# Performance work log

Hardware: AMD Instinct MI355X
Metric: run time of the kernel (lower is better)

## Reference

```python
import jax, jax.numpy as jnp
import numpy as np

D_ATOM, D_MODEL, H = 128, 512, 4
D_H = D_ATOM // H
D_FF = 4 * D_ATOM
EPS = 1e-5


def _ln(x, g, b):
    m = jnp.mean(x, axis=-1, keepdims=True)
    v = jnp.mean((x - m) ** 2, axis=-1, keepdims=True)
    return (x - m) / jnp.sqrt(v + EPS) * g + b


def setup_inputs() -> dict:
    key = jax.random.key(0)
    ks = jax.random.split(key, 20)
    B, N_ATOM, N_PAIRS, N_TOK = 2, 2048, 16384, 512
    c_atom = jax.random.normal(ks[0], (B, N_ATOM, D_ATOM), dtype=jnp.float32)
    p_lm = jax.random.normal(ks[1], (B, N_PAIRS, 16), dtype=jnp.float32)
    p_lm_idx = jax.random.randint(ks[2], (B, N_PAIRS, 2), 0, N_ATOM, dtype=jnp.int32)
    token_idx = jnp.sort(jax.random.randint(ks[3], (B, N_ATOM), 0, N_TOK, dtype=jnp.int32), axis=-1)
    s = 0.05
    w = lambda k, sh: jax.random.normal(k, sh, dtype=jnp.float32) * s
    return {
        'c_atom': c_atom, 'p_lm': p_lm, 'p_lm_idx': p_lm_idx,
        'token_idx': token_idx, 'n_tokens': N_TOK,
        'ln_attn_g': jnp.ones((D_ATOM,), jnp.float32), 'ln_attn_b': jnp.zeros((D_ATOM,), jnp.float32),
        'w_q': w(ks[4], (D_ATOM, D_ATOM)), 'w_k': w(ks[5], (D_ATOM, D_ATOM)),
        'w_v': w(ks[6], (D_ATOM, D_ATOM)), 'w_g': w(ks[7], (D_ATOM, D_ATOM)),
        'w_o': w(ks[8], (D_ATOM, D_ATOM)),
        'pb_w': w(ks[9], (16, H)), 'pb_b': jnp.zeros((H,), jnp.float32),
        'ln_ff_g': jnp.ones((D_ATOM,), jnp.float32), 'ln_ff_b': jnp.zeros((D_ATOM,), jnp.float32),
        'sw_w1': w(ks[10], (D_ATOM, D_FF)), 'sw_w2': w(ks[11], (D_ATOM, D_FF)),
        'sw_w3': w(ks[12], (D_FF, D_ATOM)),
        'tok_w': w(ks[13], (D_ATOM, D_MODEL)), 'tok_b': jnp.zeros((D_MODEL,), jnp.float32),
    }


def reference(c_atom, p_lm, p_lm_idx, token_idx, n_tokens,
              ln_attn_g, ln_attn_b, w_q, w_k, w_v, w_g, w_o, pb_w, pb_b,
              ln_ff_g, ln_ff_b, sw_w1, sw_w2, sw_w3, tok_w, tok_b):
    B, N, _ = c_atom.shape
    q_n = _ln(c_atom, ln_attn_g, ln_attn_b)
    Q = (q_n @ w_q).reshape(B, N, H, D_H)
    K = (q_n @ w_k).reshape(B, N, H, D_H)
    V = (q_n @ w_v).reshape(B, N, H, D_H)
    G = q_n @ w_g  # (B, N, d_atom)

    scores = jnp.einsum('bihd,bjhd->bhij', Q, K) / jnp.sqrt(jnp.float32(D_H))

    bias = p_lm @ pb_w + pb_b  # (B, P, H)
    def scat(src, dst, b_):
        return jnp.zeros((H, N, N), b_.dtype).at[:, src, dst].set(b_.T)
    pair_bias = jax.vmap(scat)(p_lm_idx[..., 0], p_lm_idx[..., 1], bias)
    scores = scores + pair_bias

    token_mask = token_idx[:, :, None] == token_idx[:, None, :]  # (B,N,N)
    scores = jnp.where(token_mask[:, None], scores, -jnp.inf)
    attn = jax.nn.softmax(scores, axis=-1)
    attn = jnp.nan_to_num(attn)

    att_out = jnp.einsum('bhij,bjhd->bihd', attn, V).reshape(B, N, D_ATOM)
    q = c_atom + jax.nn.sigmoid(G) * (att_out @ w_o)
    h = _ln(q, ln_ff_g, ln_ff_b)
    q = q + (jax.nn.silu(h @ sw_w1) * (h @ sw_w2)) @ sw_w3
    atom_feat = q @ tok_w + tok_b  # (B, N, d_model)

    seg = (token_idx + jnp.arange(B, dtype=token_idx.dtype)[:, None] * n_tokens).reshape(-1)
    sums = jax.ops.segment_sum(atom_feat.reshape(B * N, D_MODEL), seg, num_segments=B * n_tokens)
    cnts = jax.ops.segment_sum(jnp.ones((B * N,), atom_feat.dtype), seg, num_segments=B * n_tokens)
    out = sums / jnp.maximum(cnts, 1.0)[:, None]
    return out.reshape(B, n_tokens, D_MODEL)
```

## Files before the change

kernel.cpp:

```cpp
#include <hip/hip_runtime.h>
#include <hip/hip_bf16.h>
#include <math.h>

#define B_     2
#define N_     2048
#define DA     128
#define H_     4
#define DH     32
#define DFF    512
#define DM     512
#define NT     512
#define NP     16384
#define MAXL   32
#define LDSP   136

typedef short bf16x8 __attribute__((ext_vector_type(8)));
typedef float f32x4  __attribute__((ext_vector_type(4)));

__device__ __forceinline__ short bf16r(float x) {
    union { float f; unsigned u; } v; v.f = x;
    unsigned r = v.u + 0x7FFFu + ((v.u >> 16) & 1u);
    return (short)(r >> 16);
}
__device__ __forceinline__ float bf2f(short h) {
    union { unsigned u; float f; } v;
    v.u = ((unsigned)(unsigned short)h) << 16;
    return v.f;
}

__global__ __launch_bounds__(1024) void setup_kernel(
        const float* __restrict__ wq, const float* __restrict__ wk,
        const float* __restrict__ wv, const float* __restrict__ wg,
        const float* __restrict__ wo, const float* __restrict__ w1,
        const float* __restrict__ w2, const float* __restrict__ w3,
        const float* __restrict__ tw, const int* __restrict__ tok,
        const int* __restrict__ pidx,
        short* __restrict__ pqkvg, short* __restrict__ pwo,
        short* __restrict__ pw12, short* __restrict__ pw3,
        short* __restrict__ ptok,
        int* __restrict__ cnt, int* __restrict__ tst,
        int* __restrict__ win) {
    __shared__ int c[1024];
    __shared__ int sb[1024];
    if (blockIdx.x < 42) {
        int gid = blockIdx.x * 1024 + threadIdx.x;
        int lane = gid & 63;
        int grp = gid >> 6;
        int quad = lane >> 4, nn = lane & 15;
        const float* src; short* dst; int stride;
        if (grp < 128) {
            int g = grp; int kt = g & 3, nt = g >> 2;
            int n = nt * 16 + nn;
            const float* w = (n < 128) ? wq : (n < 256) ? wk : (n < 384) ? wv : wg;
            src = w + (kt * 32 + quad * 8) * 128 + (n & 127);
            dst = pqkvg + (g * 64 + lane) * 8;
            stride = 128;
        } else if (grp < 160) {
            int g = grp - 128; int kt = g & 3, nt = g >> 2;
            src = wo + (kt * 32 + quad * 8) * 128 + nt * 16 + nn;
            dst = pwo + (g * 64 + lane) * 8;
            stride = 128;
        } else if (grp < 416) {
            int g = grp - 160; int kt = g & 3, nt = g >> 2;
            int n = nt * 16 + nn;
            src = ((n & 1) ? w2 : w1) + (kt * 32 + quad * 8) * 512 + (n >> 1);
            dst = pw12 + (g * 64 + lane) * 8;
            stride = 512;
        } else if (grp < 544) {
            int g = grp - 416; int kt = g & 15, nt = g >> 4;
            src = w3 + (kt * 32 + quad * 8) * 128 + nt * 16 + nn;
            dst = pw3 + (g * 64 + lane) * 8;
            stride = 128;
        } else {
            int g = grp - 544; int kt = g & 3, nt = g >> 2;
            src = tw + (kt * 32 + quad * 8) * 512 + nt * 16 + nn;
            dst = ptok + (g * 64 + lane) * 8;
            stride = 512;
        }
#pragma unroll
        for (int j = 0; j < 8; j++) dst[j] = bf16r(src[j * stride]);
    } else if (blockIdx.x == 42) {
        int tid = threadIdx.x;
        c[tid] = 0;
        __syncthreads();
#pragma unroll
        for (int i = 0; i < 4; i++) {
            int idx = tid + i * 1024;
            int b = idx >> 11;
            atomicAdd(&c[b * NT + tok[idx]], 1);
        }
        __syncthreads();
        int t = tid & (NT - 1);
        int v = c[tid];
        int* cur = c;
        int* alt = sb;
        for (int d = 1; d < NT; d <<= 1) {
            int y = cur[tid];
            if (t >= d) y += cur[tid - d];
            alt[tid] = y;
            __syncthreads();
            int* tmp = cur; cur = alt; alt = tmp;
        }
        tst[tid] = cur[tid] - v;
        cnt[tid] = v;
    } else {
        int p = (blockIdx.x - 43) * 1024 + threadIdx.x;
        int b = p >> 14, pp = p & (NP - 1);
        int src = pidx[p * 2], dst = pidx[p * 2 + 1];
        if (tok[b * N_ + src] == tok[b * N_ + dst])
            atomicMax(&win[(b * N_ + src) * MAXL + (dst & 31)], pp + 1);
    }
}

__device__ __forceinline__ void ln_to_lds(const float* __restrict__ x,
                                          const float* __restrict__ g,
                                          const float* __restrict__ b,
                                          short* __restrict__ lds) {
    int t = threadIdx.x;
    int row = t >> 2, sub = t & 3;
    const float* xr = x + row * DA + sub * 32;
    float4 v[8];
    float s = 0.f, sq = 0.f;
#pragma unroll
    for (int i = 0; i < 8; i++) {
        v[i] = *(const float4*)(xr + i * 4);
        s  += v[i].x + v[i].y + v[i].z + v[i].w;
        sq += v[i].x * v[i].x + v[i].y * v[i].y + v[i].z * v[i].z + v[i].w * v[i].w;
    }
    s += __shfl_xor(s, 1); sq += __shfl_xor(sq, 1);
    s += __shfl_xor(s, 2); sq += __shfl_xor(sq, 2);
    float mean = s * (1.f / 128.f);
    float var = sq * (1.f / 128.f) - mean * mean;
    float inv = rsqrtf(var + 1e-5f);
    const float* gp = g + sub * 32;
    const float* bp = b + sub * 32;
    short* dst = lds + row * LDSP + sub * 32;
#pragma unroll
    for (int i = 0; i < 8; i++) {
        dst[i * 4 + 0] = bf16r((v[i].x - mean) * inv * gp[i * 4 + 0] + bp[i * 4 + 0]);
        dst[i * 4 + 1] = bf16r((v[i].y - mean) * inv * gp[i * 4 + 1] + bp[i * 4 + 1]);
        dst[i * 4 + 2] = bf16r((v[i].z - mean) * inv * gp[i * 4 + 2] + bp[i * 4 + 2]);
        dst[i * 4 + 3] = bf16r((v[i].w - mean) * inv * gp[i * 4 + 3] + bp[i * 4 + 3]);
    }
}

template<int K, int NTT>
__device__ __forceinline__ void gemm_lds(const short* __restrict__ Alds,
                                         const short* __restrict__ Bp,
                                         int nt0, int lane, f32x4* acc) {
    constexpr int KT = K / 32;
    const short* arow = Alds + (lane & 15) * LDSP + (lane >> 4) * 8;
    const short* bbase = Bp + nt0 * KT * 512 + lane * 8;
#pragma unroll
    for (int kt = 0; kt < KT; kt++) {
        bf16x8 a = *(const bf16x8*)(arow + kt * 32);
#pragma unroll
        for (int nt = 0; nt < NTT; nt++) {
            bf16x8 b = *(const bf16x8*)(bbase + (nt * KT + kt) * 512);
            acc[nt] = __builtin_amdgcn_mfma_f32_16x16x32_bf16(a, b, acc[nt], 0, 0, 0);
        }
    }
}

template<int K, int NTT>
__device__ __forceinline__ void gemm_glb(const short* __restrict__ A,
                                         const short* __restrict__ Bp,
                                         int m0, int nt0, int lane, f32x4* acc) {
    constexpr int KT = K / 32;
    const short* arow = A + (m0 + (lane & 15)) * K + (lane >> 4) * 8;
    const short* bbase = Bp + nt0 * KT * 512 + lane * 8;
#pragma unroll
    for (int kt = 0; kt < KT; kt++) {
        bf16x8 a = *(const bf16x8*)(arow + kt * 32);
#pragma unroll
        for (int nt = 0; nt < NTT; nt++) {
            bf16x8 b = *(const bf16x8*)(bbase + (nt * KT + kt) * 512);
            acc[nt] = __builtin_amdgcn_mfma_f32_16x16x32_bf16(a, b, acc[nt], 0, 0, 0);
        }
    }
}

__global__ __launch_bounds__(256) void lnqkvg_mfma(const float* __restrict__ c_atom,
                                                   const float* __restrict__ lg,
                                                   const float* __restrict__ lb,
                                                   const short* __restrict__ Bp,
                                                   float* __restrict__ out) {
    __shared__ short alds[64 * LDSP];
    int base = blockIdx.x * 64;
    ln_to_lds(c_atom + base * DA, lg, lb, alds);
    __syncthreads();
    int lane = threadIdx.x & 63;
    int wave = threadIdx.x >> 6;
    int nt0 = blockIdx.y * 8;
    f32x4 acc[8];
#pragma unroll
    for (int i = 0; i < 8; i++)
#pragma unroll
        for (int r = 0; r < 4; r++) acc[i][r] = 0.f;
    gemm_lds<128, 8>(alds + wave * 16 * LDSP, Bp, nt0, lane, acc);
    int r0 = base + wave * 16 + ((lane >> 4) << 2);
    int cc = lane & 15;
#pragma unroll
    for (int nt = 0; nt < 8; nt++) {
        int col = (nt0 + nt) * 16 + cc;
#pragma unroll
        for (int r = 0; r < 4; r++) out[(r0 + r) * 512 + col] = acc[nt][r];
    }
}

__global__ __launch_bounds__(128) void attn_kernel(const float* __restrict__ qkvg,
                                                   const int* __restrict__ tok,
                                                   const int* __restrict__ tst,
                                                   const int* __restrict__ cnt,
                                                   const int* __restrict__ winner,
                                                   const float* __restrict__ plm,
                                                   const float* __restrict__ pbw,
                                                   const float* __restrict__ pbb,
                                                   short* __restrict__ atth) {
    __shared__ float sc[H_][MAXL];
    int blk = blockIdx.x;
    int b = blk >> 11;
    int h = threadIdx.x >> 5, d = threadIdx.x & 31;
    int t = tok[blk];
    int start = tst[b * NT + t];
    int L = cnt[b * NT + t];
    if (L > MAXL) L = MAXL;
    float qv = qkvg[blk * 512 + h * DH + d];
    const float scale = 0.17677669529663687f;
    for (int jj = 0; jj < L; jj++) {
        int j = b * N_ + start + jj;
        float kv = qkvg[j * 512 + 128 + h * DH + d];
        float s = qv * kv;
#pragma unroll
        for (int m = 16; m; m >>= 1) s += __shfl_xor(s, m, 32);
        s *= scale;
        int pp1 = winner[blk * MAXL + ((start + jj) & 31)];
        if (pp1 > 0) {
            const float* pl = plm + (b * NP + pp1 - 1) * 16;
            float bsum = pbb[h];
#pragma unroll
            for (int f = 0; f < 16; f++) bsum += pl[f] * pbw[f * H_ + h];
            s += bsum;
        }
        if (d == 0) sc[h][jj] = s;
    }
    __syncthreads();
    float mx = -1e30f;
    for (int jj = 0; jj < L; jj++) mx = fmaxf(mx, sc[h][jj]);
    float denom = 0.f, acc = 0.f;
    for (int jj = 0; jj < L; jj++) {
        float pj = expf(sc[h][jj] - mx);
        denom += pj;
        acc += pj * qkvg[(b * N_ + start + jj) * 512 + 256 + h * DH + d];
    }
    atth[blk * DA + h * DH + d] = bf16r(acc / denom);
}

__global__ __launch_bounds__(256) void oplnffn1_mfma(const short* __restrict__ atth,
                                                     const short* __restrict__ pwo,
                                                     const float* __restrict__ qkvg,
                                                     const float* __restrict__ c_atom,
                                                     const float* __restrict__ lg,
                                                     const float* __restrict__ lb,
                                                     const short* __restrict__ pw12,
                                                     float* __restrict__ qbuf,
                                                     short* __restrict__ u) {
    __shared__ short alds[64 * LDSP];
    int lane = threadIdx.x & 63;
    int wave = threadIdx.x >> 6;
    int base = blockIdx.x * 64;
    int m0 = base + wave * 16;
    int quad = lane >> 4, cc = lane & 15;

    f32x4 acc[8];
#pragma unroll
    for (int i = 0; i < 8; i++)
#pragma unroll
        for (int r = 0; r < 4; r++) acc[i][r] = 0.f;
    gemm_glb<128, 8>(atth, pwo, m0, 0, lane, acc);

    float rsum[4], rsq[4];
#pragma unroll
    for (int r = 0; r < 4; r++) {
        int row = m0 + quad * 4 + r;
        float s = 0.f, sq = 0.f;
#pragma unroll
        for (int nt = 0; nt < 8; nt++) {
            int col = nt * 16 + cc;
            float g = qkvg[row * 512 + 384 + col];
            float sg = 1.f / (1.f + expf(-g));
            float val = c_atom[row * DA + col] + sg * acc[nt][r];
            acc[nt][r] = val;
            s += val; sq += val * val;
            if (blockIdx.y == 0) qbuf[row * DA + col] = val;
        }
        rsum[r] = s; rsq[r] = sq;
    }
#pragma unroll
    for (int m = 1; m < 16; m <<= 1) {
#pragma unroll
        for (int r = 0; r < 4; r++) {
            rsum[r] += __shfl_xor(rsum[r], m);
            rsq[r]  += __shfl_xor(rsq[r], m);
        }
    }
#pragma unroll
    for (int r = 0; r < 4; r++) {
        float mean = rsum[r] * (1.f / 128.f);
        float var = rsq[r] * (1.f / 128.f) - mean * mean;
        float inv = rsqrtf(var + 1e-5f);
        int lrow = wave * 16 + quad * 4 + r;
#pragma unroll
        for (int nt = 0; nt < 8; nt++) {
            int col = nt * 16 + cc;
            alds[lrow * LDSP + col] = bf16r((acc[nt][r] - mean) * inv * lg[col] + lb[col]);
        }
    }
    __syncthreads();

    int nt0 = blockIdx.y * 16;
    f32x4 acc2[16];
#pragma unroll
    for (int i = 0; i < 16; i++)
#pragma unroll
        for (int r = 0; r < 4; r++) acc2[i][r] = 0.f;
    gemm_lds<128, 16>(alds + wave * 16 * LDSP, pw12, nt0, lane, acc2);
    int r0 = m0 + quad * 4;
#pragma unroll
    for (int nt = 0; nt < 16; nt++) {
        int col8 = (nt0 + nt) * 8 + (cc >> 1);
#pragma unroll
        for (int r = 0; r < 4; r++) {
            float v = acc2[nt][r];
            float p = __shfl_xor(v, 1);
            if (!(lane & 1)) {
                float sil = v / (1.f + expf(-v));
                u[(r0 + r) * DFF + col8] = bf16r(sil * p);
            }
        }
    }
}

__global__ __launch_bounds__(128) void ffn2_mfma(const short* __restrict__ u,
                                                 const short* __restrict__ Bp,
                                                 const float* __restrict__ qbuf,
                                                 short* __restrict__ q2h) {
    int lane = threadIdx.x & 63;
    int m0 = blockIdx.x * 32 + (threadIdx.x >> 6) * 16;
    int nt0 = blockIdx.y * 4;
    f32x4 acc[4];
#pragma unroll
    for (int i = 0; i < 4; i++)
#pragma unroll
        for (int r = 0; r < 4; r++) acc[i][r] = 0.f;
    gemm_glb<512, 4>(u, Bp, m0, nt0, lane, acc);
    int r0 = m0 + ((lane >> 4) << 2);
    int cc = lane & 15;
#pragma unroll
    for (int nt = 0; nt < 4; nt++) {
        int col = (nt0 + nt) * 16 + cc;
#pragma unroll
        for (int r = 0; r < 4; r++) {
            int row = r0 + r;
            q2h[row * DA + col] = bf16r(qbuf[row * DA + col] + acc[nt][r]);
        }
    }
}

__global__ __launch_bounds__(256) void tokmean_mfma(const short* __restrict__ q2h,
                                                    const int* __restrict__ tst,
                                                    const int* __restrict__ cnt,
                                                    const short* __restrict__ Bp,
                                                    const float* __restrict__ tb,
                                                    float* __restrict__ out) {
    __shared__ short alds[64 * LDSP];
    int tid = threadIdx.x;
    int tt = tid >> 2, sub = tid & 3;
    int token = blockIdx.x * 64 + tt;
    int start = tst[token], n = cnt[token];
    int b = token >> 9;
    float accm[32];
#pragma unroll
    for (int i = 0; i < 32; i++) accm[i] = 0.f;
    for (int a = 0; a < n; a++) {
        const short* rp = q2h + (b * N_ + start + a) * DA + sub * 32;
#pragma unroll
        for (int v8 = 0; v8 < 4; v8++) {
            bf16x8 v = *(const bf16x8*)(rp + v8 * 8);
#pragma unroll
            for (int j = 0; j < 8; j++) accm[v8 * 8 + j] += bf2f(v[j]);
        }
    }
    float inv = (n > 0) ? 1.f / (float)n : 0.f;
    short* dst = alds + tt * LDSP + sub * 32;
#pragma unroll
    for (int i = 0; i < 32; i++) dst[i] = bf16r(accm[i] * inv);
    __syncthreads();

    int lane = tid & 63;
    int wave = tid >> 6;
    int nt0 = blockIdx.y * 4;
    f32x4 acc[4];
#pragma unroll
    for (int i = 0; i < 4; i++)
#pragma unroll
        for (int r = 0; r < 4; r++) acc[i][r] = 0.f;
    gemm_lds<128, 4>(alds + wave * 16 * LDSP, Bp, nt0, lane, acc);
    int r0 = blockIdx.x * 64 + wave * 16 + ((lane >> 4) << 2);
    int cc = lane & 15;
#pragma unroll
    for (int nt = 0; nt < 4; nt++) {
        int col = (nt0 + nt) * 16 + cc;
        float bv = tb[col];
#pragma unroll
        for (int r = 0; r < 4; r++) out[(size_t)(r0 + r) * DM + col] = acc[nt][r] + bv;
    }
}

extern "C" void kernel_launch(void* const* d_in, const int* in_sizes, int n_in,
                              void* d_out, int out_size, void* d_ws, size_t ws_size,
                              hipStream_t stream) {
    const float* c_atom  = (const float*)d_in[0];
    const float* p_lm    = (const float*)d_in[1];
    const int*   p_idx   = (const int*)d_in[2];
    const int*   tok     = (const int*)d_in[3];
    const float* ln_a_g  = (const float*)d_in[5];
    const float* ln_a_b  = (const float*)d_in[6];
    const float* w_q     = (const float*)d_in[7];
    const float* w_k     = (const float*)d_in[8];
    const float* w_v     = (const float*)d_in[9];
    const float* w_g     = (const float*)d_in[10];
    const float* w_o     = (const float*)d_in[11];
    const float* pb_w    = (const float*)d_in[12];
    const float* pb_b    = (const float*)d_in[13];
    const float* ln_f_g  = (const float*)d_in[14];
    const float* ln_f_b  = (const float*)d_in[15];
    const float* sw_w1   = (const float*)d_in[16];
    const float* sw_w2   = (const float*)d_in[17];
    const float* sw_w3   = (const float*)d_in[18];
    const float* tok_w   = (const float*)d_in[19];
    const float* tok_b   = (const float*)d_in[20];
    float* out = (float*)d_out;

    float* ws = (float*)d_ws;
    int*   cnt   = (int*)ws;
    int*   tst   = cnt + 1024;
    int*   win   = tst + 1024;
    short* pqkvg = (short*)(win + 131072);
    short* pwo   = pqkvg + 65536;
    short* pw12  = pwo + 16384;
    short* pw3   = pw12 + 131072;
    short* ptok  = pw3 + 65536;
    short* atth  = ptok + 65536;
    float* qbuf  = (float*)(atth + 524288);
    float* qkvg  = qbuf + 524288;
    short* uh    = (short*)(qkvg + 2097152);
    short* q2h   = atth;

    setup_kernel<<<75, 1024, 0, stream>>>(w_q, w_k, w_v, w_g, w_o, sw_w1, sw_w2,
                                          sw_w3, tok_w, tok, p_idx,
                                          pqkvg, pwo, pw12, pw3, ptok,
                                          cnt, tst, win);

    lnqkvg_mfma<<<dim3(64, 4), 256, 0, stream>>>(c_atom, ln_a_g, ln_a_b, pqkvg, qkvg);

    attn_kernel<<<B_ * N_, 128, 0, stream>>>(qkvg, tok, tst, cnt, win,
                                             p_lm, pb_w, pb_b, atth);

    oplnffn1_mfma<<<dim3(64, 4), 256, 0, stream>>>(atth, pwo, qkvg, c_atom,
                                                   ln_f_g, ln_f_b, pw12, qbuf, uh);

    ffn2_mfma<<<dim3(128, 2), 128, 0, stream>>>(uh, pw3, qbuf, q2h);

    tokmean_mfma<<<dim3(16, 8), 256, 0, stream>>>(q2h, tst, cnt, ptok, tok_b, out);
}
```

Before: 163.5 us.

## Move attention LN into setup, batch attention loads, retile ffn2, prefetch tokmean

The attention LayerNorm moves into the setup kernel as extra blocks that write a bf16 normalized buffer, so the QKVG GEMM reads A straight from global memory instead of normalizing once per column-block. The attention kernel now loads K values and winner indices eight at a time, and V values eight at a time, to raise memory-level parallelism. ffn2 uses half as many output tiles per block and twice as many blocks. tokmean software-prefetches the next atom row. The cost is an extra bf16 buffer round trip through global memory and more control flow.

```diff
diff --git a/kernel.cpp b/kernel.cpp
--- a/kernel.cpp
+++ b/kernel.cpp
@@ -35,9 +35,11 @@
         const float* __restrict__ w2, const float* __restrict__ w3,
         const float* __restrict__ tw, const int* __restrict__ tok,
         const int* __restrict__ pidx,
+        const float* __restrict__ c_atom, const float* __restrict__ lng,
+        const float* __restrict__ lnb,
         short* __restrict__ pqkvg, short* __restrict__ pwo,
         short* __restrict__ pw12, short* __restrict__ pw3,
-        short* __restrict__ ptok,
+        short* __restrict__ ptok, short* __restrict__ hln,
         int* __restrict__ cnt, int* __restrict__ tst,
         int* __restrict__ win) {
     __shared__ int c[1024];
@@ -103,44 +105,40 @@
         }
         tst[tid] = cur[tid] - v;
         cnt[tid] = v;
-    } else {
+    } else if (blockIdx.x < 75) {
         int p = (blockIdx.x - 43) * 1024 + threadIdx.x;
         int b = p >> 14, pp = p & (NP - 1);
         int src = pidx[p * 2], dst = pidx[p * 2 + 1];
         if (tok[b * N_ + src] == tok[b * N_ + dst])
             atomicMax(&win[(b * N_ + src) * MAXL + (dst & 31)], pp + 1);
-    }
-}
-
-__device__ __forceinline__ void ln_to_lds(const float* __restrict__ x,
-                                          const float* __restrict__ g,
-                                          const float* __restrict__ b,
-                                          short* __restrict__ lds) {
-    int t = threadIdx.x;
-    int row = t >> 2, sub = t & 3;
-    const float* xr = x + row * DA + sub * 32;
-    float4 v[8];
-    float s = 0.f, sq = 0.f;
-#pragma unroll
-    for (int i = 0; i < 8; i++) {
-        v[i] = *(const float4*)(xr + i * 4);
-        s  += v[i].x + v[i].y + v[i].z + v[i].w;
-        sq += v[i].x * v[i].x + v[i].y * v[i].y + v[i].z * v[i].z + v[i].w * v[i].w;
-    }
-    s += __shfl_xor(s, 1); sq += __shfl_xor(sq, 1);
-    s += __shfl_xor(s, 2); sq += __shfl_xor(sq, 2);
-    float mean = s * (1.f / 128.f);
-    float var = sq * (1.f / 128.f) - mean * mean;
-    float inv = rsqrtf(var + 1e-5f);
-    const float* gp = g + sub * 32;
-    const float* bp = b + sub * 32;
-    short* dst = lds + row * LDSP + sub * 32;
-#pragma unroll
-    for (int i = 0; i < 8; i++) {
-        dst[i * 4 + 0] = bf16r((v[i].x - mean) * inv * gp[i * 4 + 0] + bp[i * 4 + 0]);
-        dst[i * 4 + 1] = bf16r((v[i].y - mean) * inv * gp[i * 4 + 1] + bp[i * 4 + 1]);
-        dst[i * 4 + 2] = bf16r((v[i].z - mean) * inv * gp[i * 4 + 2] + bp[i * 4 + 2]);
-        dst[i * 4 + 3] = bf16r((v[i].w - mean) * inv * gp[i * 4 + 3] + bp[i * 4 + 3]);
+    } else {
+        int t = threadIdx.x;
+        int rowg = (blockIdx.x - 75) * 256 + (t >> 2);
+        int sub = t & 3;
+        const float* xr = c_atom + rowg * DA + sub * 32;
+        float4 v[8];
+        float s = 0.f, sq = 0.f;
+#pragma unroll
+        for (int i = 0; i < 8; i++) {
+            v[i] = *(const float4*)(xr + i * 4);
+            s  += v[i].x + v[i].y + v[i].z + v[i].w;
+            sq += v[i].x * v[i].x + v[i].y * v[i].y + v[i].z * v[i].z + v[i].w * v[i].w;
+        }
+        s += __shfl_xor(s, 1); sq += __shfl_xor(sq, 1);
+        s += __shfl_xor(s, 2); sq += __shfl_xor(sq, 2);
+        float mean = s * (1.f / 128.f);
+        float var = sq * (1.f / 128.f) - mean * mean;
+        float inv = rsqrtf(var + 1e-5f);
+        const float* gp = lng + sub * 32;
+        const float* bp = lnb + sub * 32;
+        short* dst = hln + rowg * DA + sub * 32;
+#pragma unroll
+        for (int i = 0; i < 8; i++) {
+            dst[i * 4 + 0] = bf16r((v[i].x - mean) * inv * gp[i * 4 + 0] + bp[i * 4 + 0]);
+            dst[i * 4 + 1] = bf16r((v[i].y - mean) * inv * gp[i * 4 + 1] + bp[i * 4 + 1]);
+            dst[i * 4 + 2] = bf16r((v[i].z - mean) * inv * gp[i * 4 + 2] + bp[i * 4 + 2]);
+            dst[i * 4 + 3] = bf16r((v[i].w - mean) * inv * gp[i * 4 + 3] + bp[i * 4 + 3]);
+        }
     }
 }
 
@@ -180,25 +178,20 @@
     }
 }
 
-__global__ __launch_bounds__(256) void lnqkvg_mfma(const float* __restrict__ c_atom,
-                                                   const float* __restrict__ lg,
-                                                   const float* __restrict__ lb,
-                                                   const short* __restrict__ Bp,
-                                                   float* __restrict__ out) {
-    __shared__ short alds[64 * LDSP];
-    int base = blockIdx.x * 64;
-    ln_to_lds(c_atom + base * DA, lg, lb, alds);
-    __syncthreads();
+__global__ __launch_bounds__(256) void qkvg_mfma(const short* __restrict__ hln,
+                                                 const short* __restrict__ Bp,
+                                                 float* __restrict__ out) {
     int lane = threadIdx.x & 63;
     int wave = threadIdx.x >> 6;
+    int m0 = blockIdx.x * 64 + wave * 16;
     int nt0 = blockIdx.y * 8;
     f32x4 acc[8];
 #pragma unroll
     for (int i = 0; i < 8; i++)
 #pragma unroll
         for (int r = 0; r < 4; r++) acc[i][r] = 0.f;
-    gemm_lds<128, 8>(alds + wave * 16 * LDSP, Bp, nt0, lane, acc);
-    int r0 = base + wave * 16 + ((lane >> 4) << 2);
+    gemm_glb<128, 8>(hln, Bp, m0, nt0, lane, acc);
+    int r0 = m0 + ((lane >> 4) << 2);
     int cc = lane & 15;
 #pragma unroll
     for (int nt = 0; nt < 8; nt++) {
@@ -226,32 +219,56 @@
     int L = cnt[b * NT + t];
     if (L > MAXL) L = MAXL;
     float qv = qkvg[blk * 512 + h * DH + d];
+    const float* kbase = qkvg + (size_t)(b * N_ + start) * 512 + 128 + h * DH + d;
+    const float* vbase = kbase + 128;
+    const int* wbase = winner + blk * MAXL;
     const float scale = 0.17677669529663687f;
-    for (int jj = 0; jj < L; jj++) {
-        int j = b * N_ + start + jj;
-        float kv = qkvg[j * 512 + 128 + h * DH + d];
-        float s = qv * kv;
-#pragma unroll
-        for (int m = 16; m; m >>= 1) s += __shfl_xor(s, m, 32);
-        s *= scale;
-        int pp1 = winner[blk * MAXL + ((start + jj) & 31)];
-        if (pp1 > 0) {
-            const float* pl = plm + (b * NP + pp1 - 1) * 16;
-            float bsum = pbb[h];
-#pragma unroll
-            for (int f = 0; f < 16; f++) bsum += pl[f] * pbw[f * H_ + h];
-            s += bsum;
-        }
-        if (d == 0) sc[h][jj] = s;
+    for (int j0 = 0; j0 < L; j0 += 8) {
+        int m = L - j0; if (m > 8) m = 8;
+        float kv[8]; int pw[8];
+#pragma unroll
+        for (int u = 0; u < 8; u++) {
+            if (u < m) {
+                kv[u] = kbase[(j0 + u) * 512];
+                pw[u] = wbase[(start + j0 + u) & 31];
+            }
+        }
+#pragma unroll
+        for (int u = 0; u < 8; u++) {
+            if (u < m) {
+                float s = qv * kv[u];
+#pragma unroll
+                for (int mm = 16; mm; mm >>= 1) s += __shfl_xor(s, mm, 32);
+                s *= scale;
+                if (pw[u] > 0) {
+                    const float* pl = plm + (size_t)(b * NP + pw[u] - 1) * 16;
+                    float bsum = pbb[h];
+#pragma unroll
+                    for (int f = 0; f < 16; f++) bsum += pl[f] * pbw[f * H_ + h];
+                    s += bsum;
+                }
+                if (d == 0) sc[h][j0 + u] = s;
+            }
+        }
     }
     __syncthreads();
     float mx = -1e30f;
     for (int jj = 0; jj < L; jj++) mx = fmaxf(mx, sc[h][jj]);
     float denom = 0.f, acc = 0.f;
-    for (int jj = 0; jj < L; jj++) {
-        float pj = expf(sc[h][jj] - mx);
-        denom += pj;
-        acc += pj * qkvg[(b * N_ + start + jj) * 512 + 256 + h * DH + d];
+    for (int j0 = 0; j0 < L; j0 += 8) {
+        int m = L - j0; if (m > 8) m = 8;
+        float vv[8];
+#pragma unroll
+        for (int u = 0; u < 8; u++)
+            if (u < m) vv[u] = vbase[(j0 + u) * 512];
+#pragma unroll
+        for (int u = 0; u < 8; u++) {
+            if (u < m) {
+                float pj = expf(sc[h][j0 + u] - mx);
+                denom += pj;
+                acc += pj * vv[u];
+            }
+        }
     }
     atth[blk * DA + h * DH + d] = bf16r(acc / denom);
 }
@@ -347,17 +364,17 @@
                                                  short* __restrict__ q2h) {
     int lane = threadIdx.x & 63;
     int m0 = blockIdx.x * 32 + (threadIdx.x >> 6) * 16;
-    int nt0 = blockIdx.y * 4;
-    f32x4 acc[4];
-#pragma unroll
-    for (int i = 0; i < 4; i++)
+    int nt0 = blockIdx.y * 2;
+    f32x4 acc[2];
+#pragma unroll
+    for (int i = 0; i < 2; i++)
 #pragma unroll
         for (int r = 0; r < 4; r++) acc[i][r] = 0.f;
-    gemm_glb<512, 4>(u, Bp, m0, nt0, lane, acc);
+    gemm_glb<512, 2>(u, Bp, m0, nt0, lane, acc);
     int r0 = m0 + ((lane >> 4) << 2);
     int cc = lane & 15;
 #pragma unroll
-    for (int nt = 0; nt < 4; nt++) {
+    for (int nt = 0; nt < 2; nt++) {
         int col = (nt0 + nt) * 16 + cc;
 #pragma unroll
         for (int r = 0; r < 4; r++) {
@@ -382,13 +399,25 @@
     float accm[32];
 #pragma unroll
     for (int i = 0; i < 32; i++) accm[i] = 0.f;
-    for (int a = 0; a < n; a++) {
-        const short* rp = q2h + (b * N_ + start + a) * DA + sub * 32;
-#pragma unroll
-        for (int v8 = 0; v8 < 4; v8++) {
-            bf16x8 v = *(const bf16x8*)(rp + v8 * 8);
-#pragma unroll
-            for (int j = 0; j < 8; j++) accm[v8 * 8 + j] += bf2f(v[j]);
+    const short* rp = q2h + (size_t)(b * N_ + start) * DA + sub * 32;
+    if (n > 0) {
+        bf16x8 v[4];
+#pragma unroll
+        for (int v8 = 0; v8 < 4; v8++) v[v8] = *(const bf16x8*)(rp + v8 * 8);
+        for (int a = 1; a <= n; a++) {
+            bf16x8 nx[4];
+            if (a < n) {
+#pragma unroll
+                for (int v8 = 0; v8 < 4; v8++) nx[v8] = *(const bf16x8*)(rp + a * DA + v8 * 8);
+            }
+#pragma unroll
+            for (int v8 = 0; v8 < 4; v8++)
+#pragma unroll
+                for (int j = 0; j < 8; j++) accm[v8 * 8 + j] += bf2f(v[v8][j]);
+            if (a < n) {
+#pragma unroll
+                for (int v8 = 0; v8 < 4; v8++) v[v8] = nx[v8];
+            }
         }
     }
     float inv = (n > 0) ? 1.f / (float)n : 0.f;
@@ -455,14 +484,16 @@
     float* qbuf  = (float*)(atth + 524288);
     float* qkvg  = qbuf + 524288;
     short* uh    = (short*)(qkvg + 2097152);
+    short* hln   = uh + 2097152;
     short* q2h   = atth;
 
-    setup_kernel<<<75, 1024, 0, stream>>>(w_q, w_k, w_v, w_g, w_o, sw_w1, sw_w2,
+    setup_kernel<<<91, 1024, 0, stream>>>(w_q, w_k, w_v, w_g, w_o, sw_w1, sw_w2,
                                           sw_w3, tok_w, tok, p_idx,
-                                          pqkvg, pwo, pw12, pw3, ptok,
+                                          c_atom, ln_a_g, ln_a_b,
+                                          pqkvg, pwo, pw12, pw3, ptok, hln,
                                           cnt, tst, win);
 
-    lnqkvg_mfma<<<dim3(64, 4), 256, 0, stream>>>(c_atom, ln_a_g, ln_a_b, pqkvg, qkvg);
+    qkvg_mfma<<<dim3(64, 4), 256, 0, stream>>>(hln, pqkvg, qkvg);
 
     attn_kernel<<<B_ * N_, 128, 0, stream>>>(qkvg, tok, tst, cnt, win,
                                              p_lm, pb_w, pb_b, atth);
@@ -470,7 +501,7 @@
     oplnffn1_mfma<<<dim3(64, 4), 256, 0, stream>>>(atth, pwo, qkvg, c_atom,
                                                    ln_f_g, ln_f_b, pw12, qbuf, uh);
 
-    ffn2_mfma<<<dim3(128, 2), 128, 0, stream>>>(uh, pw3, qbuf, q2h);
+    ffn2_mfma<<<dim3(128, 4), 128, 0, stream>>>(uh, pw3, qbuf, q2h);
 
     tokmean_mfma<<<dim3(16, 8), 256, 0, stream>>>(q2h, tst, cnt, ptok, tok_b, out);
 }
```

Result: slower. 167.6 us (+2.5%).
